# Optimization experiments

Measured on AMD Instinct MI355X. Metric: run time of the kernel, lower is better.

The kernel has to match this reference:

```python
import jax, jax.numpy as jnp
import numpy as np
import math

B, N, DIM = 8, 4096, 768
H, D = 12, 64
STAGES = 3
LN_EPS = 1e-5

def _ln(x, g, b):
    mu = jnp.mean(x, axis=-1, keepdims=True)
    var = jnp.mean(jnp.square(x - mu), axis=-1, keepdims=True)
    return (x - mu) * jax.lax.rsqrt(var + LN_EPS) * g + b

def _mlp(x, W, b, g, be):
    return jax.nn.gelu(_ln(x @ W + b, g, be), approximate=False)

def setup_inputs() -> dict:
    key = jax.random.key(0)
    ks = jax.random.split(key, 16)
    s = lambda i, shape, sc: jax.random.normal(ks[i], shape, jnp.float32) * sc
    return {
        "x": s(0, (B, N, DIM), 1.0),
        "Wq": s(1, (DIM, H * D), DIM ** -0.5),
        "Wk": s(2, (DIM, H * D), DIM ** -0.5),
        "Wv": s(3, (DIM, H * D), DIM ** -0.5),
        "pool_W": s(4, (STAGES, D, D), D ** -0.5),
        "pool_b": jnp.zeros((STAGES, D), jnp.float32),
        "pool_g": jnp.ones((STAGES, D), jnp.float32),
        "pool_be": jnp.zeros((STAGES, D), jnp.float32),
        "exp_W": s(5, (STAGES, D, D), D ** -0.5),
        "exp_b": jnp.zeros((STAGES, D), jnp.float32),
        "exp_g": jnp.ones((STAGES, D), jnp.float32),
        "exp_be": jnp.zeros((STAGES, D), jnp.float32),
        "Wo": s(6, (H * D, DIM), (H * D) ** -0.5),
        "bo": jnp.zeros((DIM,), jnp.float32),
    }

def reference(x, Wq, Wk, Wv, pool_W, pool_b, pool_g, pool_be,
              exp_W, exp_b, exp_g, exp_be, Wo, bo):
    b, n, _ = x.shape
    # project and split heads -> (b, h, n, d)
    def heads(y):
        return y.reshape(b, n, H, D).transpose(0, 2, 1, 3)
    q = heads(x @ Wq)
    k = heads(x @ Wk)
    v = heads(x @ Wv)
    fmap = lambda t: jax.nn.elu(t) + 1.0
    q = fmap(q)
    k = fmap(k)

    kc, vc = k, v
    for i in range(STAGES):
        s = kc.shape[2]
        if s > 1:
            pad = (-s) % 2
            if pad:
                kc = jnp.pad(kc, ((0, 0), (0, 0), (0, pad), (0, 0)))
                vc = jnp.pad(vc, ((0, 0), (0, 0), (0, pad), (0, 0)))
            kc = kc.reshape(b, H, -1, 2, D).mean(axis=3)
            kc = _mlp(kc, pool_W[i], pool_b[i], pool_g[i], pool_be[i])
            vc = vc.reshape(b, H, -1, 2, D).mean(axis=3)

    kc = kc / math.sqrt(kc.shape[2])
    kv = jnp.einsum('bhnd,bhne->bhde', kc, vc)       # (b,h,d,d)
    out = jnp.einsum('bhnd,bhde->bhne', q, kv)       # (b,h,n,d)
    k_sum = kc.sum(axis=2, keepdims=True)            # (b,h,1,d)
    q_k_sum = jnp.sum(q * k_sum, axis=-1, keepdims=True)  # (b,h,n,1)
    out = out / (q_k_sum + 1e-6)

    for i in reversed(range(STAGES)):
        out = _mlp(out, exp_W[i], exp_b[i], exp_g[i], exp_be[i])

    out = out.transpose(0, 2, 1, 3).reshape(b, n, H * D)
    return out @ Wo + bo
```

## Files before the change

kernel.cpp:

```cpp
#include <hip/hip_runtime.h>
#include <math.h>

#define B_   8
#define N_   4096
#define DIM_ 768
#define H_   12
#define D_   64

typedef unsigned short ushort_t;
typedef unsigned int uint_t;
typedef __attribute__((ext_vector_type(8))) short short8;
typedef __attribute__((ext_vector_type(4))) float f32x4;

__device__ __forceinline__ float gelu_exact(float z) {
  const float ax = fabsf(z) * 0.70710678118654752440f;
  const float t  = __builtin_amdgcn_rcpf(1.f + 0.3275911f * ax);
  float poly = ((((1.061405429f * t - 1.453152027f) * t + 1.421413741f) * t
                 - 0.284496736f) * t + 0.254829592f) * t;
  const float erfax = 1.f - poly * __expf(-ax * ax);
  const float erfv = __builtin_copysignf(erfax, z);
  return 0.5f * z * (1.f + erfv);
}

__device__ __forceinline__ ushort_t f2bf(float f) {
  union { float f; unsigned u; } x; x.f = f;
  unsigned r = x.u + 0x7FFFu + ((x.u >> 16) & 1u);
  return (ushort_t)(r >> 16);
}

__device__ __forceinline__ float bf2f(ushort_t h) {
  union { unsigned u; float f; } x; x.u = ((unsigned)h) << 16;
  return x.f;
}

__device__ __forceinline__ void gl_lds16(const ushort_t* g, ushort_t* l) {
  __builtin_amdgcn_global_load_lds(
      (const __attribute__((address_space(1))) void*)g,
      (__attribute__((address_space(3))) void*)l, 16, 0, 0);
}

__global__ __launch_bounds__(256) void transpose_w_bf16(
    const float* __restrict__ src, ushort_t* __restrict__ dst)
{
  __shared__ float t[32][33];
  const int lx = threadIdx.x & 31, ly = threadIdx.x >> 5;
  const int bx = blockIdx.x * 32;
  const int by = blockIdx.y * 32;
  #pragma unroll
  for (int j = 0; j < 32; j += 8)
    t[ly + j][lx] = src[(size_t)(by + ly + j) * 768 + bx + lx];
  __syncthreads();
  #pragma unroll
  for (int j = 0; j < 32; j += 8)
    dst[(size_t)(bx + ly + j) * 768 + by + lx] = f2bf(t[lx][ly + j]);
}

__global__ __launch_bounds__(256) void transpose64_bf16(
    const float* __restrict__ pW, const float* __restrict__ eW,
    ushort_t* __restrict__ dst)
{
  const int m = blockIdx.x;
  const float* src = (m < 3) ? (pW + m * 4096) : (eW + (m - 3) * 4096);
  ushort_t* o = dst + m * 4096;
  for (int i = threadIdx.x; i < 4096; i += 256) {
    const int r = i >> 6, c = i & 63;
    o[c * 64 + r] = f2bf(src[r * 64 + c]);
  }
}

__global__ __launch_bounds__(256) void conv_f32_bf16(
    const float* __restrict__ src, ushort_t* __restrict__ dst)
{
  const int i = blockIdx.x * 256 + threadIdx.x;
  float4 f = ((const float4*)src)[i];
  ushort4 o;
  o.x = f2bf(f.x); o.y = f2bf(f.y); o.z = f2bf(f.z); o.w = f2bf(f.w);
  ((ushort4*)dst)[i] = o;
}

__global__ __launch_bounds__(256) void pool8_x(
    const ushort_t* __restrict__ xb, ushort_t* __restrict__ x8)
{
  const int idx = blockIdx.x * 256 + threadIdx.x;
  const int r = idx / 96, gc = idx - r * 96;
  const ushort_t* p = xb + (size_t)(8 * r) * 768 + gc * 8;
  float s[8] = {};
  #pragma unroll
  for (int j = 0; j < 8; ++j) {
    short8 v = *(const short8*)(p + (size_t)j * 768);
    #pragma unroll
    for (int e = 0; e < 8; ++e) s[e] += bf2f((ushort_t)v[e]);
  }
  short8 o;
  #pragma unroll
  for (int e = 0; e < 8; ++e) o[e] = (short)f2bf(0.125f * s[e]);
  *(short8*)(x8 + (size_t)r * 768 + gc * 8) = o;
}

#define GEMM_MAINLOOP(A, Bt, K)                                               \
  __shared__ ushort_t As[128 * 32];                                           \
  __shared__ ushort_t Bs[128 * 32];                                           \
  const int tid = threadIdx.x;                                                \
  const int nwg_ = (int)(gridDim.x * gridDim.y);                              \
  const int wgid0_ = (int)(blockIdx.y * gridDim.x + blockIdx.x);              \
  const int wgid_ = (wgid0_ & 7) * (nwg_ >> 3) + (wgid0_ >> 3);               \
  const int row0 = (wgid_ / (int)gridDim.x) * 128;                            \
  const int col0 = (wgid_ % (int)gridDim.x) * 128;                            \
  const int sr = tid >> 2;                                                    \
  const int sk = (tid & 3) * 8;                                               \
  const ushort_t* Ag0 = (A) + (size_t)(row0 + sr) * (K) + sk;                 \
  const ushort_t* Ag1 = Ag0 + (size_t)64 * (K);                               \
  const ushort_t* Bg0 = (Bt) + (size_t)(col0 + sr) * (K) + sk;                \
  const ushort_t* Bg1 = Bg0 + (size_t)64 * (K);                               \
  ushort_t* Asw = As + (tid >> 6) * 512;                                      \
  ushort_t* Bsw = Bs + (tid >> 6) * 512;                                      \
  const int w = tid >> 6, lane = tid & 63;                                    \
  const int wm = w >> 1, wn = w & 1;                                          \
  const int qd = lane >> 4, l15 = lane & 15;                                  \
  const int aoff = (wm * 64 + l15) * 32 + qd * 8;                             \
  const int boff = (wn * 64 + l15) * 32 + qd * 8;                             \
  f32x4 acc[4][4] = {};                                                       \
  for (int k0 = 0; k0 < (K); k0 += 32) {                                      \
    __syncthreads();                                                          \
    gl_lds16(Ag0 + k0, Asw);                                                  \
    gl_lds16(Ag1 + k0, Asw + 2048);                                           \
    gl_lds16(Bg0 + k0, Bsw);                                                  \
    gl_lds16(Bg1 + k0, Bsw + 2048);                                           \
    __syncthreads();                                                          \
    short8 af[4], bfr[4];                                                     \
    _Pragma("unroll")                                                         \
    for (int mt = 0; mt < 4; ++mt) af[mt] = *(const short8*)&As[aoff + mt * 512]; \
    _Pragma("unroll")                                                         \
    for (int nt = 0; nt < 4; ++nt) bfr[nt] = *(const short8*)&Bs[boff + nt * 512]; \
    _Pragma("unroll")                                                         \
    for (int mt = 0; mt < 4; ++mt)                                            \
      _Pragma("unroll")                                                       \
      for (int nt = 0; nt < 4; ++nt)                                          \
        acc[mt][nt] = __builtin_amdgcn_mfma_f32_16x16x32_bf16(                \
            af[mt], bfr[nt], acc[mt][nt], 0, 0, 0);                           \
  }

__global__ __launch_bounds__(256) void gemm_qkv(
    const ushort_t* __restrict__ A, const ushort_t* __restrict__ Bt,
    ushort_t* __restrict__ qo, ushort_t* __restrict__ ko)
{
  GEMM_MAINLOOP(A, Bt, 768)
  const int sel = col0 / 768;
  const int colbase = (col0 % 768) + wn * 64;
  ushort_t* o = (sel == 0) ? qo : ko;
  #pragma unroll
  for (int mt = 0; mt < 4; ++mt) {
    #pragma unroll
    for (int nt = 0; nt < 4; ++nt) {
      const int cg = colbase + nt * 16 + l15;
      #pragma unroll
      for (int r = 0; r < 4; ++r) {
        const int rg = row0 + wm * 64 + mt * 16 + qd * 4 + r;
        const float vv = acc[mt][nt][r];
        const float e = (vv > 0.f) ? vv + 1.f : __expf(vv);
        o[(size_t)rg * 768 + cg] = f2bf(e);
      }
    }
  }
}

__global__ __launch_bounds__(256) void gemm_v(
    const ushort_t* __restrict__ A, const ushort_t* __restrict__ Bt,
    float* __restrict__ vco)
{
  GEMM_MAINLOOP(A, Bt, 768)
  #pragma unroll
  for (int mt = 0; mt < 4; ++mt) {
    #pragma unroll
    for (int nt = 0; nt < 4; ++nt) {
      const int cg = col0 + wn * 64 + nt * 16 + l15;
      const int hh = cg >> 6, d = cg & 63;
      #pragma unroll
      for (int r = 0; r < 4; ++r) {
        const int rg = row0 + wm * 64 + mt * 16 + qd * 4 + r;
        const int b = rg >> 9, n = rg & 511;
        vco[(((size_t)b * 12 + hh) * 512 + n) * 64 + d] = acc[mt][nt][r];
      }
    }
  }
}

__global__ __launch_bounds__(256) void gemm_out(
    const ushort_t* __restrict__ A, const ushort_t* __restrict__ Bt,
    const float* __restrict__ bo, float* __restrict__ C)
{
  GEMM_MAINLOOP(A, Bt, 768)
  #pragma unroll
  for (int mt = 0; mt < 4; ++mt) {
    #pragma unroll
    for (int nt = 0; nt < 4; ++nt) {
      const int cg = col0 + wn * 64 + nt * 16 + l15;
      #pragma unroll
      for (int r = 0; r < 4; ++r) {
        const int rg = row0 + wm * 64 + mt * 16 + qd * 4 + r;
        C[(size_t)rg * 768 + cg] = acc[mt][nt][r] + bo[cg];
      }
    }
  }
}

__global__ __launch_bounds__(256) void pool_mfma(
    const ushort_t* __restrict__ in, ushort_t* __restrict__ out,
    int n_out, long h_stride, int ts, long in_bs, long out_bs,
    const ushort_t* __restrict__ Wt, const float* __restrict__ bias,
    const float* __restrict__ g, const float* __restrict__ be)
{
  __shared__ ushort_t Wl[64 * 72];
  __shared__ ushort_t tl[128 * 72];
  const int tid = threadIdx.x;
  const int h = blockIdx.y;
  const int bb = blockIdx.z;
  const int row0 = blockIdx.x * 128;
  in  += (size_t)bb * in_bs;
  out += (size_t)bb * out_bs;

  {
    const uint_t* ws = (const uint_t*)Wt;
    for (int i = tid; i < 2048; i += 256) {
      const int r = i >> 5, c = i & 31;
      ((uint_t*)(Wl + r * 72))[c] = ws[i];
    }
  }
  #pragma unroll
  for (int j = 0; j < 4; ++j) {
    const int idx = j * 256 + tid;
    const int rl = idx >> 3, ch = idx & 7;
    const ushort_t* p = in + (size_t)h * h_stride + (size_t)(2 * (row0 + rl)) * ts + ch * 8;
    short8 a = *(const short8*)p;
    short8 b2 = *(const short8*)(p + ts);
    short8 o;
    #pragma unroll
    for (int e = 0; e < 8; ++e)
      o[e] = (short)f2bf(0.5f * (bf2f((ushort_t)a[e]) + bf2f((ushort_t)b2[e])));
    *(short8*)&tl[rl * 72 + ch * 8] = o;
  }
  __syncthreads();

  const int w = tid >> 6, lane = tid & 63;
  const int quad = lane >> 4, l15 = lane & 15;

  float bv[4], gv[4], bev[4];
  #pragma unroll
  for (int nt = 0; nt < 4; ++nt) {
    const int c = nt * 16 + l15;
    bv[nt] = bias[c]; gv[nt] = g[c]; bev[nt] = be[c];
  }
  f32x4 a2[2][4];
  #pragma unroll
  for (int mt = 0; mt < 2; ++mt)
    #pragma unroll
    for (int nt = 0; nt < 4; ++nt)
      a2[mt][nt] = f32x4{bv[nt], bv[nt], bv[nt], bv[nt]};

  #pragma unroll
  for (int ks = 0; ks < 2; ++ks) {
    short8 af[2], bfr[4];
    #pragma unroll
    for (int mt = 0; mt < 2; ++mt)
      af[mt] = *(const short8*)&tl[(w * 32 + mt * 16 + l15) * 72 + ks * 32 + quad * 8];
    #pragma unroll
    for (int nt = 0; nt < 4; ++nt)
      bfr[nt] = *(const short8*)&Wl[(nt * 16 + l15) * 72 + ks * 32 + quad * 8];
    #pragma unroll
    for (int mt = 0; mt < 2; ++mt)
      #pragma unroll
      for (int nt = 0; nt < 4; ++nt)
        a2[mt][nt] = __builtin_amdgcn_mfma_f32_16x16x32_bf16(af[mt], bfr[nt], a2[mt][nt], 0, 0, 0);
  }

  #pragma unroll
  for (int mt = 0; mt < 2; ++mt)
    #pragma unroll
    for (int r = 0; r < 4; ++r) {
      float sum = a2[mt][0][r] + a2[mt][1][r] + a2[mt][2][r] + a2[mt][3][r];
      #pragma unroll
      for (int m = 1; m < 16; m <<= 1) sum += __shfl_xor(sum, m, 64);
      const float mu = sum * 0.015625f;
      float dv[4], var = 0.f;
      #pragma unroll
      for (int nt = 0; nt < 4; ++nt) { dv[nt] = a2[mt][nt][r] - mu; var += dv[nt] * dv[nt]; }
      #pragma unroll
      for (int m = 1; m < 16; m <<= 1) var += __shfl_xor(var, m, 64);
      const float rstd = rsqrtf(var * 0.015625f + 1e-5f);
      const int rg = row0 + w * 32 + mt * 16 + quad * 4 + r;
      #pragma unroll
      for (int nt = 0; nt < 4; ++nt) {
        const float z = dv[nt] * rstd * gv[nt] + bev[nt];
        out[((size_t)h * n_out + rg) * 64 + nt * 16 + l15] = f2bf(gelu_exact(z));
      }
    }
}

__global__ __launch_bounds__(256) void kv_part_kernel(
    const ushort_t* __restrict__ kc, const float* __restrict__ vc,
    float* __restrict__ kvp, float* __restrict__ ksp)
{
  __shared__ float ks[32 * 64];
  __shared__ float vs[32 * 64];
  const int tid = threadIdx.x;
  const int h = blockIdx.x;
  const int c = blockIdx.y;
  const int bb = blockIdx.z;
  kc  += (size_t)bb * 393216;
  vc  += (size_t)bb * 393216;
  kvp += (size_t)bb * 786432;
  ksp += (size_t)bb * 12288;
  const ushort_t* kp = kc + ((size_t)h * 512 + c * 32) * 64;
  const float* vp = vc + ((size_t)h * 512 + c * 32) * 64;
  #pragma unroll
  for (int i = 0; i < 2; ++i) {
    ushort4 u = ((const ushort4*)kp)[tid + 256 * i];
    float4 f; f.x = bf2f(u.x); f.y = bf2f(u.y); f.z = bf2f(u.z); f.w = bf2f(u.w);
    ((float4*)ks)[tid + 256 * i] = f;
    ((float4*)vs)[tid + 256 * i] = ((const float4*)vp)[tid + 256 * i];
  }
  __syncthreads();

  const int e = tid & 63;
  const int dg = tid >> 6;
  float acc[16] = {};
  float accs = 0.f;
  for (int nn = 0; nn < 32; ++nn) {
    const float vv = vs[nn * 64 + e];
    #pragma unroll
    for (int j = 0; j < 16; ++j)
      acc[j] += ks[nn * 64 + dg * 16 + j] * vv;
    if (tid < 64) accs += ks[nn * 64 + tid];
  }
  float* o = kvp + ((size_t)h * 16 + c) * 4096;
  #pragma unroll
  for (int j = 0; j < 16; ++j)
    o[(dg * 16 + j) * 64 + e] = acc[j];
  if (tid < 64) ksp[(h * 16 + c) * 64 + tid] = accs;
}

__global__ __launch_bounds__(256) void kv_reduce_t(
    const float* __restrict__ kvp, const float* __restrict__ ksp,
    ushort_t* __restrict__ kvxT)
{
  const int bb = blockIdx.y;
  kvp  += (size_t)bb * 786432;
  ksp  += (size_t)bb * 12288;
  kvxT += (size_t)bb * 61440;
  const int idx = blockIdx.x * 256 + threadIdx.x;
  const int h = idx / 5120;
  const int rem = idx - h * 5120;
  const int er = rem >> 6, d = rem & 63;
  const float scale = 0.044194173824159216f;
  float val = 0.f;
  if (er < 64) {
    float s = 0.f;
    #pragma unroll
    for (int c = 0; c < 16; ++c) s += kvp[((size_t)h * 16 + c) * 4096 + d * 64 + er];
    val = s * scale;
  } else if (er == 64) {
    float s = 0.f;
    #pragma unroll
    for (int c = 0; c < 16; ++c) s += ksp[(h * 16 + c) * 64 + d];
    val = s * scale;
  }
  kvxT[idx] = f2bf(val);
}

__global__ __launch_bounds__(256) void attn_exp_mfma(
    const ushort_t* __restrict__ q16, const ushort_t* __restrict__ kvxT,
    const ushort_t* __restrict__ eWt,
    const float* __restrict__ eb, const float* __restrict__ eg,
    const float* __restrict__ ebe, ushort_t* __restrict__ out16)
{
  __shared__ ushort_t Wl[3 * 64 * 72];
  __shared__ ushort_t tl[128 * 72];
  const int tid = threadIdx.x;
  const int h = blockIdx.y;
  const int bb = blockIdx.z;
  const int row0 = blockIdx.x * 128;
  q16   += (size_t)bb * 3145728;
  out16 += (size_t)bb * 3145728;
  const ushort_t* kvx = kvxT + (size_t)bb * 61440 + (size_t)h * 5120;

  {
    const uint_t* ws = (const uint_t*)eWt;
    for (int i = tid; i < 6144; i += 256) {
      const int s = i >> 11, rem = i & 2047, r = rem >> 5, c = rem & 31;
      ((uint_t*)(Wl + (s * 64 + r) * 72))[c] = ws[i];
    }
  }
  __syncthreads();

  const int w = tid >> 6, lane = tid & 63;
  const int quad = lane >> 4, l15 = lane & 15;

  f32x4 acc[2][5] = {};
  #pragma unroll
  for (int ks = 0; ks < 2; ++ks) {
    short8 af[2], bfr[5];
    #pragma unroll
    for (int mt = 0; mt < 2; ++mt) {
      const int rg = row0 + w * 32 + mt * 16 + l15;
      af[mt] = *(const short8*)(q16 + (size_t)rg * 768 + h * 64 + ks * 32 + quad * 8);
    }
    #pragma unroll
    for (int nt = 0; nt < 5; ++nt)
      bfr[nt] = *(const short8*)(kvx + (nt * 16 + l15) * 64 + ks * 32 + quad * 8);
    #pragma unroll
    for (int mt = 0; mt < 2; ++mt)
      #pragma unroll
      for (int nt = 0; nt < 5; ++nt)
        acc[mt][nt] = __builtin_amdgcn_mfma_f32_16x16x32_bf16(af[mt], bfr[nt], acc[mt][nt], 0, 0, 0);
  }

  float t[2][4][4];
  #pragma unroll
  for (int mt = 0; mt < 2; ++mt)
    #pragma unroll
    for (int r = 0; r < 4; ++r) {
      const float den = __shfl(acc[mt][4][r], lane & 48, 64) + 1e-6f;
      const float inv = __builtin_amdgcn_rcpf(den);
      #pragma unroll
      for (int nt = 0; nt < 4; ++nt)
        t[mt][nt][r] = acc[mt][nt][r] * inv;
    }

  for (int s = 2; s >= 0; --s) {
    __syncthreads();
    #pragma unroll
    for (int mt = 0; mt < 2; ++mt)
      #pragma unroll
      for (int nt = 0; nt < 4; ++nt)
        #pragma unroll
        for (int r = 0; r < 4; ++r)
          tl[(w * 32 + mt * 16 + quad * 4 + r) * 72 + nt * 16 + l15] = f2bf(t[mt][nt][r]);
    __syncthreads();

    float bv[4], gv[4], bev[4];
    #pragma unroll
    for (int nt = 0; nt < 4; ++nt) {
      const int c = s * 64 + nt * 16 + l15;
      bv[nt] = eb[c]; gv[nt] = eg[c]; bev[nt] = ebe[c];
    }
    f32x4 a2[2][4];
    #pragma unroll
    for (int mt = 0; mt < 2; ++mt)
      #pragma unroll
      for (int nt = 0; nt < 4; ++nt)
        a2[mt][nt] = f32x4{bv[nt], bv[nt], bv[nt], bv[nt]};

    #pragma unroll
    for (int ks = 0; ks < 2; ++ks) {
      short8 af[2], bfr[4];
      #pragma unroll
      for (int mt = 0; mt < 2; ++mt)
        af[mt] = *(const short8*)&tl[(w * 32 + mt * 16 + l15) * 72 + ks * 32 + quad * 8];
      #pragma unroll
      for (int nt = 0; nt < 4; ++nt)
        bfr[nt] = *(const short8*)&Wl[(s * 64 + nt * 16 + l15) * 72 + ks * 32 + quad * 8];
      #pragma unroll
      for (int mt = 0; mt < 2; ++mt)
        #pragma unroll
        for (int nt = 0; nt < 4; ++nt)
          a2[mt][nt] = __builtin_amdgcn_mfma_f32_16x16x32_bf16(af[mt], bfr[nt], a2[mt][nt], 0, 0, 0);
    }

    #pragma unroll
    for (int mt = 0; mt < 2; ++mt)
      #pragma unroll
      for (int r = 0; r < 4; ++r) {
        float sum = a2[mt][0][r] + a2[mt][1][r] + a2[mt][2][r] + a2[mt][3][r];
        #pragma unroll
        for (int m = 1; m < 16; m <<= 1) sum += __shfl_xor(sum, m, 64);
        const float mu = sum * 0.015625f;
        float dv[4], var = 0.f;
        #pragma unroll
        for (int nt = 0; nt < 4; ++nt) { dv[nt] = a2[mt][nt][r] - mu; var += dv[nt] * dv[nt]; }
        #pragma unroll
        for (int m = 1; m < 16; m <<= 1) var += __shfl_xor(var, m, 64);
        const float rstd = rsqrtf(var * 0.015625f + 1e-5f);
        #pragma unroll
        for (int nt = 0; nt < 4; ++nt) {
          const float z = dv[nt] * rstd * gv[nt] + bev[nt];
          t[mt][nt][r] = gelu_exact(z);
        }
      }
  }

  #pragma unroll
  for (int mt = 0; mt < 2; ++mt)
    #pragma unroll
    for (int nt = 0; nt < 4; ++nt)
      #pragma unroll
      for (int r = 0; r < 4; ++r) {
        const int rg = row0 + w * 32 + mt * 16 + quad * 4 + r;
        out16[(size_t)rg * 768 + h * 64 + nt * 16 + l15] = f2bf(t[mt][nt][r]);
      }
}

extern "C" void kernel_launch(void* const* d_in, const int* in_sizes, int n_in,
                              void* d_out, int out_size, void* d_ws, size_t ws_size,
                              hipStream_t stream)
{
  const float* x   = (const float*)d_in[0];
  const float* Wq  = (const float*)d_in[1];
  const float* Wk  = (const float*)d_in[2];
  const float* Wv  = (const float*)d_in[3];
  const float* pW  = (const float*)d_in[4];
  const float* pb  = (const float*)d_in[5];
  const float* pg  = (const float*)d_in[6];
  const float* pbe = (const float*)d_in[7];
  const float* eW  = (const float*)d_in[8];
  const float* eb  = (const float*)d_in[9];
  const float* eg  = (const float*)d_in[10];
  const float* ebe = (const float*)d_in[11];
  const float* Wo  = (const float*)d_in[12];
  const float* bo  = (const float*)d_in[13];
  float* outp = (float*)d_out;

  unsigned char* wsb = (unsigned char*)d_ws;
  ushort_t* WqkvT = (ushort_t*)(wsb + 0);
  ushort_t* WoT   = (ushort_t*)(wsb + 3538944);
  ushort_t* Wt6   = (ushort_t*)(wsb + 4718592);
  const size_t CB   = 4767744;
  const size_t PERB = 26861568;

  int NB;
  if      (ws_size >= CB + 8 * PERB) NB = 8;
  else if (ws_size >= CB + 4 * PERB) NB = 4;
  else if (ws_size >= CB + 2 * PERB) NB = 2;
  else if (ws_size >= CB + 1 * PERB) NB = 1;
  else return;

  unsigned char* cb = wsb + CB;
  ushort_t* xb16 = (ushort_t*)(cb);
  ushort_t* q16  = (ushort_t*)(cb + (size_t)NB *  6291456);
  ushort_t* k16  = (ushort_t*)(cb + (size_t)NB * 12582912);
  float*    vc   = (float*)   (cb + (size_t)NB * 18874368);
  ushort_t* kc_a = (ushort_t*)(cb + (size_t)NB * 20447232);
  ushort_t* kc_b = (ushort_t*)(cb + (size_t)NB * 23592960);
  ushort_t* kc_c = (ushort_t*)(cb + (size_t)NB * 25165824);
  ushort_t* kvxT = (ushort_t*)(cb + (size_t)NB * 25952256);
  ushort_t* x8   = (ushort_t*)(cb + (size_t)NB * 26075136);
  float* kvp = (float*)k16;
  float* ksp = (float*)((unsigned char*)k16 + (size_t)NB * 3145728);
  ushort_t* ao16 = xb16;

  const ushort_t* pWt = Wt6;
  const ushort_t* eWt = Wt6 + 3 * 4096;
  const size_t SB = (size_t)N_ * DIM_;

  transpose_w_bf16<<<dim3(24, 24), 256, 0, stream>>>(Wq, WqkvT);
  transpose_w_bf16<<<dim3(24, 24), 256, 0, stream>>>(Wk, WqkvT + 768 * 768);
  transpose_w_bf16<<<dim3(24, 24), 256, 0, stream>>>(Wv, WqkvT + 2 * 768 * 768);
  transpose_w_bf16<<<dim3(24, 24), 256, 0, stream>>>(Wo, WoT);
  transpose64_bf16<<<6, 256, 0, stream>>>(pW, eW, Wt6);

  const ushort_t* WvT = WqkvT + 2 * 768 * 768;

  for (int b0 = 0; b0 < B_; b0 += NB) {
    const float* xc = x + (size_t)b0 * SB;
    float* oc = outp + (size_t)b0 * SB;

    conv_f32_bf16<<<NB * 3072, 256, 0, stream>>>(xc, xb16);
    pool8_x<<<NB * 192, 256, 0, stream>>>(xb16, x8);
    gemm_qkv<<<dim3(12, NB * 32), 256, 0, stream>>>(xb16, WqkvT, q16, k16);
    gemm_v<<<dim3(6, NB * 4), 256, 0, stream>>>(x8, WvT, vc);

    pool_mfma<<<dim3(16, 12, NB), 256, 0, stream>>>(k16, kc_a, 2048, 64L, 768,
        3145728L, 1572864L, pWt, pb, pg, pbe);
    pool_mfma<<<dim3(8, 12, NB), 256, 0, stream>>>(kc_a, kc_b, 1024, 131072L, 64,
        1572864L, 786432L, pWt + 4096, pb + 64, pg + 64, pbe + 64);
    pool_mfma<<<dim3(4, 12, NB), 256, 0, stream>>>(kc_b, kc_c, 512, 65536L, 64,
        786432L, 393216L, pWt + 8192, pb + 128, pg + 128, pbe + 128);

    kv_part_kernel<<<dim3(12, 16, NB), 256, 0, stream>>>(kc_c, vc, kvp, ksp);
    kv_reduce_t<<<dim3(240, NB), 256, 0, stream>>>(kvp, ksp, kvxT);

    attn_exp_mfma<<<dim3(32, 12, NB), 256, 0, stream>>>(q16, kvxT, eWt,
                                                        eb, eg, ebe, ao16);

    gemm_out<<<dim3(6, NB * 32), 256, 0, stream>>>(ao16, WoT, bo, oc);
  }
}
```

Before: 586.5 us.

## Fuse three pooling MLP stages and kv partial product into one kernel

Replaces three pool_mfma launches and kv_part_kernel with a single kernel that keeps each 128-row chunk of a head in shared memory across all three pool+MLP stages and then computes the kv and k-sum partials directly. This removes the intermediate global writes and reads of kc_a/kc_b/kc_c and three kernel launches. In exchange the later stages leave most waves idle, since stage 2 uses one tile per wave and stage 3 runs only on two waves, and each block uses more shared memory, which may lower occupancy.

After: 581.3 us. No clear change (-0.9%).

```diff
diff --git a/kernel.cpp b/kernel.cpp
--- a/kernel.cpp
+++ b/kernel.cpp
@@ -204,121 +204,140 @@
   }
 }
 
-__global__ __launch_bounds__(256) void pool_mfma(
-    const ushort_t* __restrict__ in, ushort_t* __restrict__ out,
-    int n_out, long h_stride, int ts, long in_bs, long out_bs,
-    const ushort_t* __restrict__ Wt, const float* __restrict__ bias,
-    const float* __restrict__ g, const float* __restrict__ be)
-{
-  __shared__ ushort_t Wl[64 * 72];
-  __shared__ ushort_t tl[128 * 72];
+__device__ __forceinline__ void mlp_stage(
+    const ushort_t* __restrict__ inb, ushort_t* __restrict__ outb,
+    const ushort_t* __restrict__ Wls, const float* __restrict__ bias,
+    const float* __restrict__ g, const float* __restrict__ be,
+    int rowbase, int ntiles, int tid)
+{
+  if (ntiles == 0) return;
+  const int lane = tid & 63, quad = lane >> 4, l15 = lane & 15;
+  float bv[4], gv[4], bev[4];
+  #pragma unroll
+  for (int nt = 0; nt < 4; ++nt) {
+    const int c = nt * 16 + l15;
+    bv[nt] = bias[c]; gv[nt] = g[c]; bev[nt] = be[c];
+  }
+  f32x4 a2[2][4];
+  #pragma unroll
+  for (int mt = 0; mt < 2; ++mt)
+    #pragma unroll
+    for (int nt = 0; nt < 4; ++nt)
+      a2[mt][nt] = f32x4{bv[nt], bv[nt], bv[nt], bv[nt]};
+
+  #pragma unroll
+  for (int ks = 0; ks < 2; ++ks) {
+    short8 af[2], bfr[4];
+    #pragma unroll
+    for (int mt = 0; mt < 2; ++mt)
+      if (mt < ntiles)
+        af[mt] = *(const short8*)&inb[(rowbase + mt * 16 + l15) * 72 + ks * 32 + quad * 8];
+    #pragma unroll
+    for (int nt = 0; nt < 4; ++nt)
+      bfr[nt] = *(const short8*)&Wls[(nt * 16 + l15) * 72 + ks * 32 + quad * 8];
+    #pragma unroll
+    for (int mt = 0; mt < 2; ++mt)
+      if (mt < ntiles)
+        #pragma unroll
+        for (int nt = 0; nt < 4; ++nt)
+          a2[mt][nt] = __builtin_amdgcn_mfma_f32_16x16x32_bf16(af[mt], bfr[nt], a2[mt][nt], 0, 0, 0);
+  }
+
+  #pragma unroll
+  for (int mt = 0; mt < 2; ++mt) {
+    if (mt >= ntiles) continue;
+    #pragma unroll
+    for (int r = 0; r < 4; ++r) {
+      float sum = a2[mt][0][r] + a2[mt][1][r] + a2[mt][2][r] + a2[mt][3][r];
+      #pragma unroll
+      for (int m = 1; m < 16; m <<= 1) sum += __shfl_xor(sum, m, 64);
+      const float mu = sum * 0.015625f;
+      float dv[4], var = 0.f;
+      #pragma unroll
+      for (int nt = 0; nt < 4; ++nt) { dv[nt] = a2[mt][nt][r] - mu; var += dv[nt] * dv[nt]; }
+      #pragma unroll
+      for (int m = 1; m < 16; m <<= 1) var += __shfl_xor(var, m, 64);
+      const float rstd = rsqrtf(var * 0.015625f + 1e-5f);
+      const int rl = rowbase + mt * 16 + quad * 4 + r;
+      #pragma unroll
+      for (int nt = 0; nt < 4; ++nt) {
+        const float z = dv[nt] * rstd * gv[nt] + bev[nt];
+        outb[rl * 72 + nt * 16 + l15] = f2bf(gelu_exact(z));
+      }
+    }
+  }
+}
+
+__device__ __forceinline__ void pool_pairs(
+    const ushort_t* __restrict__ inb, ushort_t* __restrict__ outb,
+    int outRows, int tid)
+{
+  for (int idx = tid; idx < outRows * 8; idx += 256) {
+    const int rl = idx >> 3, ch = idx & 7;
+    short8 a = *(const short8*)&inb[(2 * rl) * 72 + ch * 8];
+    short8 b = *(const short8*)&inb[(2 * rl + 1) * 72 + ch * 8];
+    short8 o;
+    #pragma unroll
+    for (int e = 0; e < 8; ++e)
+      o[e] = (short)f2bf(0.5f * (bf2f((ushort_t)a[e]) + bf2f((ushort_t)b[e])));
+    *(short8*)&outb[rl * 72 + ch * 8] = o;
+  }
+}
+
+__global__ __launch_bounds__(256) void pool_kv_fused(
+    const ushort_t* __restrict__ k16, const float* __restrict__ vc,
+    const ushort_t* __restrict__ pWt,
+    const float* __restrict__ pb, const float* __restrict__ pg,
+    const float* __restrict__ pbe,
+    float* __restrict__ kvp, float* __restrict__ ksp)
+{
+  __shared__ ushort_t Wl[3 * 64 * 72];
+  __shared__ ushort_t bufA[128 * 72];
+  __shared__ ushort_t bufB[128 * 72];
+  __shared__ float    vs[32 * 64];
   const int tid = threadIdx.x;
+  const int x = blockIdx.x;
   const int h = blockIdx.y;
   const int bb = blockIdx.z;
-  const int row0 = blockIdx.x * 128;
-  in  += (size_t)bb * in_bs;
-  out += (size_t)bb * out_bs;
+  const ushort_t* kin = k16 + (size_t)bb * 3145728;
+  const float* vp = vc + (size_t)bb * 393216 + ((size_t)h * 512 + x * 32) * 64;
 
   {
-    const uint_t* ws = (const uint_t*)Wt;
-    for (int i = tid; i < 2048; i += 256) {
-      const int r = i >> 5, c = i & 31;
-      ((uint_t*)(Wl + r * 72))[c] = ws[i];
+    const uint_t* ws = (const uint_t*)pWt;
+    for (int i = tid; i < 6144; i += 256) {
+      const int s = i >> 11, rem = i & 2047, r = rem >> 5, c = rem & 31;
+      ((uint_t*)(Wl + (s * 64 + r) * 72))[c] = ws[i];
     }
   }
   #pragma unroll
   for (int j = 0; j < 4; ++j) {
     const int idx = j * 256 + tid;
     const int rl = idx >> 3, ch = idx & 7;
-    const ushort_t* p = in + (size_t)h * h_stride + (size_t)(2 * (row0 + rl)) * ts + ch * 8;
+    const ushort_t* p = kin + (size_t)h * 64 + (size_t)(2 * (x * 128 + rl)) * 768 + ch * 8;
     short8 a = *(const short8*)p;
-    short8 b2 = *(const short8*)(p + ts);
+    short8 b2 = *(const short8*)(p + 768);
     short8 o;
     #pragma unroll
     for (int e = 0; e < 8; ++e)
       o[e] = (short)f2bf(0.5f * (bf2f((ushort_t)a[e]) + bf2f((ushort_t)b2[e])));
-    *(short8*)&tl[rl * 72 + ch * 8] = o;
-  }
-  __syncthreads();
-
-  const int w = tid >> 6, lane = tid & 63;
-  const int quad = lane >> 4, l15 = lane & 15;
-
-  float bv[4], gv[4], bev[4];
-  #pragma unroll
-  for (int nt = 0; nt < 4; ++nt) {
-    const int c = nt * 16 + l15;
-    bv[nt] = bias[c]; gv[nt] = g[c]; bev[nt] = be[c];
-  }
-  f32x4 a2[2][4];
-  #pragma unroll
-  for (int mt = 0; mt < 2; ++mt)
-    #pragma unroll
-    for (int nt = 0; nt < 4; ++nt)
-      a2[mt][nt] = f32x4{bv[nt], bv[nt], bv[nt], bv[nt]};
-
-  #pragma unroll
-  for (int ks = 0; ks < 2; ++ks) {
-    short8 af[2], bfr[4];
-    #pragma unroll
-    for (int mt = 0; mt < 2; ++mt)
-      af[mt] = *(const short8*)&tl[(w * 32 + mt * 16 + l15) * 72 + ks * 32 + quad * 8];
-    #pragma unroll
-    for (int nt = 0; nt < 4; ++nt)
-      bfr[nt] = *(const short8*)&Wl[(nt * 16 + l15) * 72 + ks * 32 + quad * 8];
-    #pragma unroll
-    for (int mt = 0; mt < 2; ++mt)
-      #pragma unroll
-      for (int nt = 0; nt < 4; ++nt)
-        a2[mt][nt] = __builtin_amdgcn_mfma_f32_16x16x32_bf16(af[mt], bfr[nt], a2[mt][nt], 0, 0, 0);
-  }
-
-  #pragma unroll
-  for (int mt = 0; mt < 2; ++mt)
-    #pragma unroll
-    for (int r = 0; r < 4; ++r) {
-      float sum = a2[mt][0][r] + a2[mt][1][r] + a2[mt][2][r] + a2[mt][3][r];
-      #pragma unroll
-      for (int m = 1; m < 16; m <<= 1) sum += __shfl_xor(sum, m, 64);
-      const float mu = sum * 0.015625f;
-      float dv[4], var = 0.f;
-      #pragma unroll
-      for (int nt = 0; nt < 4; ++nt) { dv[nt] = a2[mt][nt][r] - mu; var += dv[nt] * dv[nt]; }
-      #pragma unroll
-      for (int m = 1; m < 16; m <<= 1) var += __shfl_xor(var, m, 64);
-      const float rstd = rsqrtf(var * 0.015625f + 1e-5f);
-      const int rg = row0 + w * 32 + mt * 16 + quad * 4 + r;
-      #pragma unroll
-      for (int nt = 0; nt < 4; ++nt) {
-        const float z = dv[nt] * rstd * gv[nt] + bev[nt];
-        out[((size_t)h * n_out + rg) * 64 + nt * 16 + l15] = f2bf(gelu_exact(z));
-      }
-    }
-}
-
-__global__ __launch_bounds__(256) void kv_part_kernel(
-    const ushort_t* __restrict__ kc, const float* __restrict__ vc,
-    float* __restrict__ kvp, float* __restrict__ ksp)
-{
-  __shared__ float ks[32 * 64];
-  __shared__ float vs[32 * 64];
-  const int tid = threadIdx.x;
-  const int h = blockIdx.x;
-  const int c = blockIdx.y;
-  const int bb = blockIdx.z;
-  kc  += (size_t)bb * 393216;
-  vc  += (size_t)bb * 393216;
-  kvp += (size_t)bb * 786432;
-  ksp += (size_t)bb * 12288;
-  const ushort_t* kp = kc + ((size_t)h * 512 + c * 32) * 64;
-  const float* vp = vc + ((size_t)h * 512 + c * 32) * 64;
-  #pragma unroll
-  for (int i = 0; i < 2; ++i) {
-    ushort4 u = ((const ushort4*)kp)[tid + 256 * i];
-    float4 f; f.x = bf2f(u.x); f.y = bf2f(u.y); f.z = bf2f(u.z); f.w = bf2f(u.w);
-    ((float4*)ks)[tid + 256 * i] = f;
+    *(short8*)&bufA[rl * 72 + ch * 8] = o;
+  }
+  #pragma unroll
+  for (int i = 0; i < 2; ++i)
     ((float4*)vs)[tid + 256 * i] = ((const float4*)vp)[tid + 256 * i];
-  }
+  __syncthreads();
+
+  const int w = tid >> 6;
+  mlp_stage(bufA, bufB, Wl, pb, pg, pbe, w * 32, 2, tid);
+  __syncthreads();
+  pool_pairs(bufB, bufA, 64, tid);
+  __syncthreads();
+  mlp_stage(bufA, bufB, Wl + 64 * 72, pb + 64, pg + 64, pbe + 64, w * 16, 1, tid);
+  __syncthreads();
+  pool_pairs(bufB, bufA, 32, tid);
+  __syncthreads();
+  mlp_stage(bufA, bufB, Wl + 128 * 72, pb + 128, pg + 128, pbe + 128,
+            w * 16, (w < 2) ? 1 : 0, tid);
   __syncthreads();
 
   const int e = tid & 63;
@@ -329,14 +348,14 @@
     const float vv = vs[nn * 64 + e];
     #pragma unroll
     for (int j = 0; j < 16; ++j)
-      acc[j] += ks[nn * 64 + dg * 16 + j] * vv;
-    if (tid < 64) accs += ks[nn * 64 + tid];
-  }
-  float* o = kvp + ((size_t)h * 16 + c) * 4096;
+      acc[j] += bf2f(bufB[nn * 72 + dg * 16 + j]) * vv;
+    if (tid < 64) accs += bf2f(bufB[nn * 72 + tid]);
+  }
+  float* o = kvp + (size_t)bb * 786432 + ((size_t)h * 16 + x) * 4096;
   #pragma unroll
   for (int j = 0; j < 16; ++j)
     o[(dg * 16 + j) * 64 + e] = acc[j];
-  if (tid < 64) ksp[(h * 16 + c) * 64 + tid] = accs;
+  if (tid < 64) ksp[(size_t)bb * 12288 + (h * 16 + x) * 64 + tid] = accs;
 }
 
 __global__ __launch_bounds__(256) void kv_reduce_t(
@@ -540,11 +559,10 @@
   float*    vc   = (float*)   (cb + (size_t)NB * 18874368);
   ushort_t* kc_a = (ushort_t*)(cb + (size_t)NB * 20447232);
   ushort_t* kc_b = (ushort_t*)(cb + (size_t)NB * 23592960);
-  ushort_t* kc_c = (ushort_t*)(cb + (size_t)NB * 25165824);
   ushort_t* kvxT = (ushort_t*)(cb + (size_t)NB * 25952256);
   ushort_t* x8   = (ushort_t*)(cb + (size_t)NB * 26075136);
-  float* kvp = (float*)k16;
-  float* ksp = (float*)((unsigned char*)k16 + (size_t)NB * 3145728);
+  float* kvp = (float*)kc_a;
+  float* ksp = (float*)kc_b;
   ushort_t* ao16 = xb16;
 
   const ushort_t* pWt = Wt6;
@@ -568,14 +586,8 @@
     gemm_qkv<<<dim3(12, NB * 32), 256, 0, stream>>>(xb16, WqkvT, q16, k16);
     gemm_v<<<dim3(6, NB * 4), 256, 0, stream>>>(x8, WvT, vc);
 
-    pool_mfma<<<dim3(16, 12, NB), 256, 0, stream>>>(k16, kc_a, 2048, 64L, 768,
-        3145728L, 1572864L, pWt, pb, pg, pbe);
-    pool_mfma<<<dim3(8, 12, NB), 256, 0, stream>>>(kc_a, kc_b, 1024, 131072L, 64,
-        1572864L, 786432L, pWt + 4096, pb + 64, pg + 64, pbe + 64);
-    pool_mfma<<<dim3(4, 12, NB), 256, 0, stream>>>(kc_b, kc_c, 512, 65536L, 64,
-        786432L, 393216L, pWt + 8192, pb + 128, pg + 128, pbe + 128);
-
-    kv_part_kernel<<<dim3(12, 16, NB), 256, 0, stream>>>(kc_c, vc, kvp, ksp);
+    pool_kv_fused<<<dim3(16, 12, NB), 256, 0, stream>>>(k16, vc, pWt,
+                                                        pb, pg, pbe, kvp, ksp);
     kv_reduce_t<<<dim3(240, NB), 256, 0, stream>>>(kvp, ksp, kvxT);
 
     attn_exp_mfma<<<dim3(32, 12, NB), 256, 0, stream>>>(q16, kvxT, eWt,
```
